# Performance work log

Hardware: AMD Instinct MI355X
Metric: run time of the kernel (lower is better)

The kernel has to match this reference:

```python
import jax, jax.numpy as jnp
import numpy as np

NUM_TOKENS = 16384
INPUT_DIM = 4096
NUM_EXPERTS = 64
TOP_K = 2


def setup_inputs() -> dict:
    key = jax.random.key(0)
    k1, k2 = jax.random.split(key)
    x = jax.random.normal(k1, (NUM_TOKENS, INPUT_DIM), dtype=jnp.float32)
    # nn.Linear default init scale ~ 1/sqrt(fan_in); keep similar magnitude
    W = jax.random.normal(k2, (NUM_EXPERTS, INPUT_DIM), dtype=jnp.float32) / jnp.sqrt(INPUT_DIM).astype(jnp.float32)
    b = jnp.zeros((NUM_EXPERTS,), dtype=jnp.float32)
    return {"x": x, "W": W, "b": b}


def reference(x, W, b):
    # gating_scores = x @ W^T + b  -> [tokens, experts]
    scores = jnp.einsum('td,ed->te', x, W) + b
    probs = jax.nn.softmax(scores, axis=1)
    top_k_values, top_k_indices = jax.lax.top_k(probs, TOP_K)
    # torch returns (indices, values) in this module's forward
    return (top_k_indices, top_k_values)
```

## Files before the change

### kernel.cpp

```cpp
#include <hip/hip_runtime.h>
#include <math.h>

#define TOKENS 16384
#define DIM    4096
#define NEXP   64
#define KSPLIT 8
#define KPW    (DIM / KSPLIT)
#define NF4    (KPW / 4)

__global__ __launch_bounds__(256)
void transpose_w(const float* __restrict__ W, float* __restrict__ Wt)
{
    const int idx = blockIdx.x * 256 + threadIdx.x;
    const int e = idx & (NEXP - 1);
    const int k = idx >> 6;
    Wt[(size_t)k * NEXP + e] = W[(size_t)e * DIM + k];
}

__global__ __launch_bounds__(512, 1)
void gating_kernel(const float* __restrict__ x,
                   const float* __restrict__ Wt,
                   const float* __restrict__ bias,
                   float* __restrict__ out)
{
    __shared__ float red[4][64][NEXP];

    const int tid  = threadIdx.x;
    const int lane = tid & 63;
    const int wid  = __builtin_amdgcn_readfirstlane(tid >> 6);
    const int tok  = blockIdx.x * 64 + lane;

    float acc[64];
    if (wid == 0) {
#pragma unroll
        for (int c = 0; c < 16; ++c) {
            const float4 bv = *(const float4*)(bias + c * 4);
            acc[c*4+0] = bv.x; acc[c*4+1] = bv.y; acc[c*4+2] = bv.z; acc[c*4+3] = bv.w;
        }
    } else {
#pragma unroll
        for (int e = 0; e < 64; ++e) acc[e] = 0.f;
    }

    const float4* xr = (const float4*)(x + (size_t)tok * DIM + wid * KPW);
    const float* wb = Wt + (size_t)(wid * KPW) * NEXP;

    float4 xv = xr[0];
    for (int i = 0; i < NF4; ++i) {
        float4 xn = xv;
        if (i + 1 < NF4) xn = xr[i + 1];
        const float* wr = wb + (size_t)i * (4 * NEXP);
#pragma unroll
        for (int kk = 0; kk < 4; ++kk) {
            const float xk = (kk == 0) ? xv.x : (kk == 1) ? xv.y
                           : (kk == 2) ? xv.z : xv.w;
            const float* wkr = wr + kk * NEXP;
#pragma unroll
            for (int e4 = 0; e4 < 16; ++e4) {
                const float4 w = *(const float4*)(wkr + e4 * 4);
                acc[e4*4+0] = fmaf(xk, w.x, acc[e4*4+0]);
                acc[e4*4+1] = fmaf(xk, w.y, acc[e4*4+1]);
                acc[e4*4+2] = fmaf(xk, w.z, acc[e4*4+2]);
                acc[e4*4+3] = fmaf(xk, w.w, acc[e4*4+3]);
            }
        }
        xv = xn;
    }

    auto lds_write = [&](int slot) {
#pragma unroll
        for (int c = 0; c < 16; ++c) {
            const int cs = c ^ (lane & 7);
            *(float4*)&red[slot][lane][cs * 4] =
                make_float4(acc[c*4], acc[c*4+1], acc[c*4+2], acc[c*4+3]);
        }
    };
    auto lds_add = [&](int slot) {
#pragma unroll
        for (int c = 0; c < 16; ++c) {
            const int cs = c ^ (lane & 7);
            const float4 v = *(const float4*)&red[slot][lane][cs * 4];
            acc[c*4+0] += v.x; acc[c*4+1] += v.y;
            acc[c*4+2] += v.z; acc[c*4+3] += v.w;
        }
    };

    if (wid >= 4) lds_write(wid - 4);
    __syncthreads();
    if (wid < 4) lds_add(wid);
    __syncthreads();
    if (wid == 2 || wid == 3) lds_write(wid - 2);
    __syncthreads();
    if (wid < 2) lds_add(wid);
    __syncthreads();
    if (wid == 1) lds_write(0);
    __syncthreads();

    if (wid == 0) {
        lds_add(0);
        float m1 = -INFINITY, m2 = -INFINITY;
        int i1 = 0, i2 = 0;
#pragma unroll
        for (int e = 0; e < 64; ++e) {
            const float v = acc[e];
            const bool gt1 = v > m1;
            const bool gt2 = v > m2;
            m2 = gt1 ? m1 : (gt2 ? v : m2);
            i2 = gt1 ? i1 : (gt2 ? e : i2);
            m1 = gt1 ? v : m1;
            i1 = gt1 ? e : i1;
        }
        float denom = 0.f;
#pragma unroll
        for (int e = 0; e < 64; ++e) denom += __expf(acc[e] - m1);
        const float inv = 1.0f / denom;
        out[2*tok + 0] = (float)i1;
        out[2*tok + 1] = (float)i2;
        out[2*TOKENS + 2*tok + 0] = inv;
        out[2*TOKENS + 2*tok + 1] = __expf(m2 - m1) * inv;
    }
}

extern "C" void kernel_launch(void* const* d_in, const int* in_sizes, int n_in,
                              void* d_out, int out_size, void* d_ws, size_t ws_size,
                              hipStream_t stream)
{
    const float* x = (const float*)d_in[0];
    const float* W = (const float*)d_in[1];
    const float* b = (const float*)d_in[2];
    float* out = (float*)d_out;
    float* Wt  = (float*)d_ws;

    transpose_w<<<dim3((DIM * NEXP) / 256), dim3(256), 0, stream>>>(W, Wt);
    gating_kernel<<<dim3(TOKENS / 64), dim3(512), 0, stream>>>(x, Wt, b, (float*)d_out);
}
```

Baseline: 500.4 us.

## Replace per-token GEMV gating with LDS-tiled split-K GEMM plus finalize kernel

```diff
diff --git a/kernel.cpp b/kernel.cpp
--- a/kernel.cpp
+++ b/kernel.cpp
@@ -4,120 +4,159 @@
 #define TOKENS 16384
 #define DIM    4096
 #define NEXP   64
-#define KSPLIT 8
-#define KPW    (DIM / KSPLIT)
-#define NF4    (KPW / 4)
+#define BT     256
+#define BK     16
+#define LSTR   20
+
+__global__ __launch_bounds__(256, 2)
+void gemm_partial(const float* __restrict__ x, const float* __restrict__ W,
+                  float* __restrict__ part, int nstep)
+{
+    __shared__ float xs [2][BT][LSTR];
+    __shared__ float wsh[2][NEXP][LSTR];
+
+    const int tid   = threadIdx.x;
+    const int tg    = blockIdx.x & 63;
+    const int ks    = blockIdx.x >> 6;
+    const int tb    = tg * BT;
+    const int kbase = ks * nstep * BK;
+
+    const int srow = tid >> 2;
+    const int sc   = (tid & 3) << 2;
+
+    const int tr = tid >> 3;
+    const int er = tid & 7;
+
+    float acc[8][8];
+#pragma unroll
+    for (int i = 0; i < 8; ++i)
+#pragma unroll
+        for (int j = 0; j < 8; ++j) acc[i][j] = 0.f;
+
+    {
+        const int k0 = kbase;
+        float4 gx0 = *(const float4*)&x[(size_t)(tb+srow      )*DIM + k0 + sc];
+        float4 gx1 = *(const float4*)&x[(size_t)(tb+srow +  64)*DIM + k0 + sc];
+        float4 gx2 = *(const float4*)&x[(size_t)(tb+srow + 128)*DIM + k0 + sc];
+        float4 gx3 = *(const float4*)&x[(size_t)(tb+srow + 192)*DIM + k0 + sc];
+        float4 gw0 = *(const float4*)&W[(size_t)srow*DIM + k0 + sc];
+        *(float4*)&xs [0][srow      ][sc] = gx0;
+        *(float4*)&xs [0][srow +  64][sc] = gx1;
+        *(float4*)&xs [0][srow + 128][sc] = gx2;
+        *(float4*)&xs [0][srow + 192][sc] = gx3;
+        *(float4*)&wsh[0][srow      ][sc] = gw0;
+    }
+    __syncthreads();
+
+    for (int s = 0; s < nstep; ++s) {
+        const int p = s & 1;
+        const bool more = (s + 1 < nstep);
+        float4 gx0, gx1, gx2, gx3, gw0;
+        if (more) {
+            const int k0 = kbase + (s + 1) * BK;
+            gx0 = *(const float4*)&x[(size_t)(tb+srow      )*DIM + k0 + sc];
+            gx1 = *(const float4*)&x[(size_t)(tb+srow +  64)*DIM + k0 + sc];
+            gx2 = *(const float4*)&x[(size_t)(tb+srow + 128)*DIM + k0 + sc];
+            gx3 = *(const float4*)&x[(size_t)(tb+srow + 192)*DIM + k0 + sc];
+            gw0 = *(const float4*)&W[(size_t)srow*DIM + k0 + sc];
+        }
+
+#pragma unroll
+        for (int kq = 0; kq < 4; ++kq) {
+            float4 xv[8], wv[8];
+#pragma unroll
+            for (int i = 0; i < 8; ++i)
+                xv[i] = *(const float4*)&xs [p][tr + 32*i][kq << 2];
+#pragma unroll
+            for (int j = 0; j < 8; ++j)
+                wv[j] = *(const float4*)&wsh[p][er +  8*j][kq << 2];
+#pragma unroll
+            for (int i = 0; i < 8; ++i)
+#pragma unroll
+                for (int j = 0; j < 8; ++j) {
+                    acc[i][j] = fmaf(xv[i].x, wv[j].x, acc[i][j]);
+                    acc[i][j] = fmaf(xv[i].y, wv[j].y, acc[i][j]);
+                    acc[i][j] = fmaf(xv[i].z, wv[j].z, acc[i][j]);
+                    acc[i][j] = fmaf(xv[i].w, wv[j].w, acc[i][j]);
+                }
+        }
+
+        if (more) {
+            const int q = p ^ 1;
+            *(float4*)&xs [q][srow      ][sc] = gx0;
+            *(float4*)&xs [q][srow +  64][sc] = gx1;
+            *(float4*)&xs [q][srow + 128][sc] = gx2;
+            *(float4*)&xs [q][srow + 192][sc] = gx3;
+            *(float4*)&wsh[q][srow      ][sc] = gw0;
+        }
+        __syncthreads();
+    }
+
+    float* pp = part + (size_t)ks * TOKENS * NEXP;
+#pragma unroll
+    for (int i = 0; i < 8; ++i) {
+        const int t = tb + tr + 32*i;
+#pragma unroll
+        for (int j = 0; j < 8; ++j)
+            pp[(size_t)t * NEXP + er + 8*j] = acc[i][j];
+    }
+}
 
 __global__ __launch_bounds__(256)
-void transpose_w(const float* __restrict__ W, float* __restrict__ Wt)
+void finalize(const float* __restrict__ part, const float* __restrict__ bias,
+              float* __restrict__ out, int ksplit)
 {
-    const int idx = blockIdx.x * 256 + threadIdx.x;
-    const int e = idx & (NEXP - 1);
-    const int k = idx >> 6;
-    Wt[(size_t)k * NEXP + e] = W[(size_t)e * DIM + k];
-}
+    const int tid = threadIdx.x;
+    const int t   = blockIdx.x * 64 + (tid >> 2);
+    const int eq  = tid & 3;
 
-__global__ __launch_bounds__(512, 1)
-void gating_kernel(const float* __restrict__ x,
-                   const float* __restrict__ Wt,
-                   const float* __restrict__ bias,
-                   float* __restrict__ out)
-{
-    __shared__ float red[4][64][NEXP];
+    float sc[16];
+#pragma unroll
+    for (int c = 0; c < 16; ++c) sc[c] = 0.f;
 
-    const int tid  = threadIdx.x;
-    const int lane = tid & 63;
-    const int wid  = __builtin_amdgcn_readfirstlane(tid >> 6);
-    const int tok  = blockIdx.x * 64 + lane;
+    for (int s = 0; s < ksplit; ++s) {
+        const float* p = part + ((size_t)s * TOKENS + t) * NEXP + eq * 16;
+#pragma unroll
+        for (int c4 = 0; c4 < 4; ++c4) {
+            const float4 v = *(const float4*)(p + c4 * 4);
+            sc[c4*4+0] += v.x; sc[c4*4+1] += v.y;
+            sc[c4*4+2] += v.z; sc[c4*4+3] += v.w;
+        }
+    }
+#pragma unroll
+    for (int c = 0; c < 16; ++c) sc[c] += bias[eq * 16 + c];
 
-    float acc[64];
-    if (wid == 0) {
+    float m1 = -INFINITY, m2 = -INFINITY;
+    int   i1 = 0, i2 = 0;
 #pragma unroll
-        for (int c = 0; c < 16; ++c) {
-            const float4 bv = *(const float4*)(bias + c * 4);
-            acc[c*4+0] = bv.x; acc[c*4+1] = bv.y; acc[c*4+2] = bv.z; acc[c*4+3] = bv.w;
-        }
-    } else {
-#pragma unroll
-        for (int e = 0; e < 64; ++e) acc[e] = 0.f;
+    for (int c = 0; c < 16; ++c) {
+        const float v = sc[c];
+        const int   e = eq * 16 + c;
+        if (v > m1)      { m2 = m1; i2 = i1; m1 = v; i1 = e; }
+        else if (v > m2) { m2 = v;  i2 = e; }
     }
 
-    const float4* xr = (const float4*)(x + (size_t)tok * DIM + wid * KPW);
-    const float* wb = Wt + (size_t)(wid * KPW) * NEXP;
-
-    float4 xv = xr[0];
-    for (int i = 0; i < NF4; ++i) {
-        float4 xn = xv;
-        if (i + 1 < NF4) xn = xr[i + 1];
-        const float* wr = wb + (size_t)i * (4 * NEXP);
 #pragma unroll
-        for (int kk = 0; kk < 4; ++kk) {
-            const float xk = (kk == 0) ? xv.x : (kk == 1) ? xv.y
-                           : (kk == 2) ? xv.z : xv.w;
-            const float* wkr = wr + kk * NEXP;
-#pragma unroll
-            for (int e4 = 0; e4 < 16; ++e4) {
-                const float4 w = *(const float4*)(wkr + e4 * 4);
-                acc[e4*4+0] = fmaf(xk, w.x, acc[e4*4+0]);
-                acc[e4*4+1] = fmaf(xk, w.y, acc[e4*4+1]);
-                acc[e4*4+2] = fmaf(xk, w.z, acc[e4*4+2]);
-                acc[e4*4+3] = fmaf(xk, w.w, acc[e4*4+3]);
-            }
-        }
-        xv = xn;
+    for (int d = 1; d <= 2; d <<= 1) {
+        const float om1 = __shfl_xor(m1, d); const int oi1 = __shfl_xor(i1, d);
+        const float om2 = __shfl_xor(m2, d); const int oi2 = __shfl_xor(i2, d);
+        if (om1 > m1 || (om1 == m1 && oi1 < i1)) { m2 = m1; i2 = i1; m1 = om1; i1 = oi1; }
+        else if (om1 > m2 || (om1 == m2 && oi1 < i2)) { m2 = om1; i2 = oi1; }
+        if (om2 > m2 || (om2 == m2 && oi2 < i2)) { m2 = om2; i2 = oi2; }
     }
 
-    auto lds_write = [&](int slot) {
+    float ds = 0.f;
 #pragma unroll
-        for (int c = 0; c < 16; ++c) {
-            const int cs = c ^ (lane & 7);
-            *(float4*)&red[slot][lane][cs * 4] =
-                make_float4(acc[c*4], acc[c*4+1], acc[c*4+2], acc[c*4+3]);
-        }
-    };
-    auto lds_add = [&](int slot) {
-#pragma unroll
-        for (int c = 0; c < 16; ++c) {
-            const int cs = c ^ (lane & 7);
-            const float4 v = *(const float4*)&red[slot][lane][cs * 4];
-            acc[c*4+0] += v.x; acc[c*4+1] += v.y;
-            acc[c*4+2] += v.z; acc[c*4+3] += v.w;
-        }
-    };
+    for (int c = 0; c < 16; ++c) ds += __expf(sc[c] - m1);
+    ds += __shfl_xor(ds, 1);
+    ds += __shfl_xor(ds, 2);
 
-    if (wid >= 4) lds_write(wid - 4);
-    __syncthreads();
-    if (wid < 4) lds_add(wid);
-    __syncthreads();
-    if (wid == 2 || wid == 3) lds_write(wid - 2);
-    __syncthreads();
-    if (wid < 2) lds_add(wid);
-    __syncthreads();
-    if (wid == 1) lds_write(0);
-    __syncthreads();
-
-    if (wid == 0) {
-        lds_add(0);
-        float m1 = -INFINITY, m2 = -INFINITY;
-        int i1 = 0, i2 = 0;
-#pragma unroll
-        for (int e = 0; e < 64; ++e) {
-            const float v = acc[e];
-            const bool gt1 = v > m1;
-            const bool gt2 = v > m2;
-            m2 = gt1 ? m1 : (gt2 ? v : m2);
-            i2 = gt1 ? i1 : (gt2 ? e : i2);
-            m1 = gt1 ? v : m1;
-            i1 = gt1 ? e : i1;
-        }
-        float denom = 0.f;
-#pragma unroll
-        for (int e = 0; e < 64; ++e) denom += __expf(acc[e] - m1);
-        const float inv = 1.0f / denom;
-        out[2*tok + 0] = (float)i1;
-        out[2*tok + 1] = (float)i2;
-        out[2*TOKENS + 2*tok + 0] = inv;
-        out[2*TOKENS + 2*tok + 1] = __expf(m2 - m1) * inv;
+    if (eq == 0) {
+        const float inv = 1.0f / ds;
+        out[2*t + 0] = (float)i1;
+        out[2*t + 1] = (float)i2;
+        out[2*TOKENS + 2*t + 0] = inv;
+        out[2*TOKENS + 2*t + 1] = __expf(m2 - m1) * inv;
     }
 }
 
@@ -128,9 +167,14 @@
     const float* x = (const float*)d_in[0];
     const float* W = (const float*)d_in[1];
     const float* b = (const float*)d_in[2];
-    float* out = (float*)d_out;
-    float* Wt  = (float*)d_ws;
+    float* out  = (float*)d_out;
+    float* part = (float*)d_ws;
 
-    transpose_w<<<dim3((DIM * NEXP) / 256), dim3(256), 0, stream>>>(W, Wt);
-    gating_kernel<<<dim3(TOKENS / 64), dim3(512), 0, stream>>>(x, Wt, b, (float*)d_out);
+    int ksplit = 8;
+    while (ksplit > 1 && ws_size < (size_t)ksplit * TOKENS * NEXP * sizeof(float))
+        ksplit >>= 1;
+    const int nstep = (DIM / ksplit) / BK;
+
+    gemm_partial<<<dim3((TOKENS / BT) * ksplit), dim3(256), 0, stream>>>(x, W, part, nstep);
+    finalize   <<<dim3(TOKENS / 64),             dim3(256), 0, stream>>>(part, b, out, ksplit);
 }
```

After: 1.058 ms. 2.12x slower.
